# Kernel tuning notes

Measured on AMD Instinct MI355X. Metric: run time of the kernel, lower is better.

## Reference

```python
import jax, jax.numpy as jnp
import numpy as np

B, H, SQ, SKV, D = 2, 16, 2048, 2048, 64
SCALE = 8  # sqrt(head_dim)


def setup_inputs() -> dict:
    key = jax.random.key(0)
    kq, kk, kv, km = jax.random.split(key, 4)
    q = jax.random.normal(kq, (B, H, SQ, D), dtype=jnp.float32)
    k = jax.random.normal(kk, (B, H, SKV, D), dtype=jnp.float32)
    v = jax.random.normal(kv, (B, H, SKV, D), dtype=jnp.float32)
    mask = jax.random.normal(km, (1, 1, SQ, SKV), dtype=jnp.float32)
    return {"q": q, "k": k, "v": v, "mask": mask, "scale": SCALE}


def reference(q, k, v, mask, scale):
    # scores: [B, H, SQ, SKV]
    scores = jnp.einsum("bhqd,bhkd->bhqk", q, k) / scale
    scores = scores + mask  # broadcast additive mask
    probs = jax.nn.softmax(scores, axis=-1)
    # hidden: [B, H, SQ, D]
    return jnp.einsum("bhqk,bhkd->bhqd", probs, v)
```

## Files before the change

### kernel.cpp

```cpp
#include <hip/hip_runtime.h>
#include <hip/hip_bf16.h>

#define NB 2
#define NH 16
#define NSQ 2048
#define NSKV 2048
#define ND 64
#define NT (NSKV / 64)
#define LOG2E 1.4426950408889634f
#define BHSTRIDE (NSKV * ND)

typedef __attribute__((ext_vector_type(8))) short bf16x8;
typedef __attribute__((ext_vector_type(4))) float f32x4;
typedef __attribute__((address_space(1))) const unsigned gas_u32;
typedef __attribute__((address_space(3))) unsigned las_u32;

__device__ __forceinline__ short f2bf(float x) {
  union { float f; unsigned u; } c; c.f = x;
  unsigned r = c.u + 0x7fffu + ((c.u >> 16) & 1u);
  return (short)(r >> 16);
}
__device__ __forceinline__ unsigned pack_bf2(float lo, float hi) {
  union { __hip_bfloat162 h; unsigned u; } c;
  c.h = __float22bfloat162_rn(float2{lo, hi});
  return c.u;
}
__device__ __forceinline__ float u2f(unsigned u) {
  union { unsigned u; float f; } c; c.u = u; return c.f;
}
__device__ __forceinline__ float exp2_fast(float x) {
#if __has_builtin(__builtin_amdgcn_exp2f)
  return __builtin_amdgcn_exp2f(x);
#else
  return exp2f(x);
#endif
}

__device__ __forceinline__ int kvmap(int x) {
  return (x & 3) | (((x >> 4) & 1) << 2) | (((x >> 2) & 1) << 3)
       | (((x >> 3) & 1) << 4) | (x & 32);
}

__global__ void prep_k(const float* __restrict__ K, short* __restrict__ Kp) {
  const int bh = blockIdx.y, tile = blockIdx.x, tid = (int)threadIdx.x;
#pragma unroll
  for (int h = 0; h < 2; ++h) {
    const int u    = tid + h * 256;
    const int nt   = u >> 7, kc = (u >> 6) & 1, lane = u & 63;
    const int prow = nt * 16 + (lane & 15);
    const float* src = K + ((size_t)bh * NSKV + tile * 64 + kvmap(prow)) * ND
                         + kc * 32 + (lane >> 4) * 8;
    float4 a = *(const float4*)src, b = *(const float4*)(src + 4);
    bf16x8 w;
    w[0]=f2bf(a.x); w[1]=f2bf(a.y); w[2]=f2bf(a.z); w[3]=f2bf(a.w);
    w[4]=f2bf(b.x); w[5]=f2bf(b.y); w[6]=f2bf(b.z); w[7]=f2bf(b.w);
    *(bf16x8*)(Kp + (size_t)bh * BHSTRIDE + (size_t)tile * 4096 + u * 8) = w;
  }
}

__global__ void prep_vt(const float* __restrict__ V, short* __restrict__ Vp) {
  __shared__ float T[64][65];
  const int kv0 = blockIdx.x * 64;
  const int bh  = blockIdx.y;
  const int t   = (int)threadIdx.x;
  const float* src = V + ((size_t)bh * NSKV + kv0) * ND;
#pragma unroll
  for (int i = 0; i < 4; ++i) {
    float4 v = *(const float4*)(src + (size_t)((t >> 4) + 16 * i) * ND + (t & 15) * 4);
    T[(t >> 4) + 16 * i][(t & 15) * 4 + 0] = v.x;
    T[(t >> 4) + 16 * i][(t & 15) * 4 + 1] = v.y;
    T[(t >> 4) + 16 * i][(t & 15) * 4 + 2] = v.z;
    T[(t >> 4) + 16 * i][(t & 15) * 4 + 3] = v.w;
  }
  __syncthreads();
  const int d = t >> 2, c = t & 3;
  bf16x8 w0, w1;
#pragma unroll
  for (int j = 0; j < 8; ++j) w0[j] = f2bf(T[c * 16 + j][d]);
#pragma unroll
  for (int j = 0; j < 8; ++j) w1[j] = f2bf(T[c * 16 + 8 + j][d]);
  const int frag  = (d >> 4) * 2 + (c >> 1);
  const int lane0 = (((2 * c) & 3) << 4) | (d & 15);
  const int lane1 = (((2 * c + 1) & 3) << 4) | (d & 15);
  short* dstb = Vp + (size_t)bh * BHSTRIDE + (size_t)blockIdx.x * 4096 + frag * 512;
  *(bf16x8*)(dstb + lane0 * 8) = w0;
  *(bf16x8*)(dstb + lane1 * 8) = w1;
}

__global__ void prep_mt(const float* __restrict__ M, unsigned short* __restrict__ Mt) {
  const int qt = blockIdx.x, kt = blockIdx.y, t = (int)threadIdx.x;
  const int rl = t >> 4, c = t & 15;
  const int row = qt * 16 + rl;
  float4 v = *(const float4*)(M + (size_t)row * NSKV + kt * 64 + c * 4);
  const int nt   = 2 * (c >> 3) + (c & 1);
  const int lq   = (c >> 1) & 3;
  const int lane = lq * 16 + rl;
  ushort4 o;
  o.x = (unsigned short)f2bf(LOG2E * v.x);
  o.y = (unsigned short)f2bf(LOG2E * v.y);
  o.z = (unsigned short)f2bf(LOG2E * v.z);
  o.w = (unsigned short)f2bf(LOG2E * v.w);
  *(ushort4*)(Mt + (((size_t)qt * 32 + kt) * 64 + lane) * 16 + nt * 4) = o;
}

__global__ __launch_bounds__(512, 4)
void attn_fwd(const float* __restrict__ Q, const short* __restrict__ Kp,
              const short* __restrict__ Vp, const unsigned short* __restrict__ Mt,
              const void* __restrict__ scale_p, float* __restrict__ O)
{
  const int lin = (int)blockIdx.x;
  const int j   = lin & 7, m = lin >> 3;
  const int qb  = 2 * j + (m & 1);
  const int bh  = m >> 1;

  const int tid = (int)threadIdx.x;
  const int wv  = tid >> 6;
  const int ln  = tid & 63;
  const int l16 = ln & 15;
  const int lq  = ln >> 4;

  float scale_v;
  {
    union { int i; float f; } u;
    u.i = ((const int*)scale_p)[0];
    float af = fabsf(u.f);
    scale_v = (af >= 1e-6f && af <= 1e6f) ? u.f : (float)u.i;
  }
  const float qmul = LOG2E / scale_v;

  const int q0 = qb * 128;
  const short* Kb = Kp + (size_t)bh * BHSTRIDE;
  const short* Vb = Vp + (size_t)bh * BHSTRIDE;

  __shared__ short Kl[2][4096];
  __shared__ short Vl[2][4096];

  bf16x8 qf[2];
  {
    const float* qrow = Q + ((size_t)bh * NSQ + q0 + wv * 16 + l16) * ND;
#pragma unroll
    for (int kc = 0; kc < 2; ++kc) {
      const float4* p = (const float4*)(qrow + kc * 32 + lq * 8);
      float4 a = p[0], b = p[1];
      bf16x8 f;
      f[0]=f2bf(a.x*qmul); f[1]=f2bf(a.y*qmul); f[2]=f2bf(a.z*qmul); f[3]=f2bf(a.w*qmul);
      f[4]=f2bf(b.x*qmul); f[5]=f2bf(b.y*qmul); f[6]=f2bf(b.z*qmul); f[7]=f2bf(b.w*qmul);
      qf[kc] = f;
    }
  }

  f32x4 oa[4];
  f32x4 lacc;
#pragma unroll
  for (int dt = 0; dt < 4; ++dt) { f32x4 z = {0.f,0.f,0.f,0.f}; oa[dt] = z; }
  { f32x4 z = {0.f,0.f,0.f,0.f}; lacc = z; }

  bf16x8 ones;
#pragma unroll
  for (int j2 = 0; j2 < 8; ++j2) ones[j2] = (short)0x3F80;

  const unsigned short* M0 = Mt + (size_t)(qb * 8 + wv) * 32768 + (size_t)ln * 16;

  union MU { uint4 q[2]; unsigned u[8]; };

  auto mload = [&](int t, MU& mu) {
    const unsigned short* p0 = M0 + (size_t)t * 1024;
    mu.q[0] = *(const uint4*)p0;
    mu.q[1] = *(const uint4*)(p0 + 8);
  };

  auto stage = [&](int t, int buf) {
    const short* ks = Kb + (size_t)t * 4096;
    const short* vs = Vb + (size_t)t * 4096;
    __builtin_amdgcn_global_load_lds((gas_u32*)(ks + wv * 512 + ln * 8),
                                     (las_u32*)&Kl[buf][wv * 512], 16, 0, 0);
    __builtin_amdgcn_global_load_lds((gas_u32*)(vs + wv * 512 + ln * 8),
                                     (las_u32*)&Vl[buf][wv * 512], 16, 0, 0);
  };

  auto tile = [&](int t, int buf, MU& mc, MU& mn) {
    if (t + 1 < NT) {
      stage(t + 1, buf ^ 1);
      mload(t + 1, mn);
    }
    bf16x8 kf[4][2], vf[4][2];
#pragma unroll
    for (int nt = 0; nt < 4; ++nt)
#pragma unroll
      for (int kc = 0; kc < 2; ++kc) {
        kf[nt][kc] = *(const bf16x8*)&Kl[buf][(nt * 2 + kc) * 512 + ln * 8];
        vf[nt][kc] = *(const bf16x8*)&Vl[buf][(nt * 2 + kc) * 512 + ln * 8];
      }
    f32x4 s[4];
    __builtin_amdgcn_s_setprio(1);
#pragma unroll
    for (int nt = 0; nt < 4; ++nt) {
      const unsigned w0 = mc.u[nt * 2], w1 = mc.u[nt * 2 + 1];
      f32x4 a;
      a[0] = u2f(w0 << 16); a[1] = u2f(w0 & 0xffff0000u);
      a[2] = u2f(w1 << 16); a[3] = u2f(w1 & 0xffff0000u);
      a = __builtin_amdgcn_mfma_f32_16x16x32_bf16(kf[nt][0], qf[0], a, 0, 0, 0);
      a = __builtin_amdgcn_mfma_f32_16x16x32_bf16(kf[nt][1], qf[1], a, 0, 0, 0);
      s[nt] = a;
    }
    __builtin_amdgcn_s_setprio(0);
#pragma unroll
    for (int nt = 0; nt < 4; ++nt) {
      s[nt][0] = exp2_fast(s[nt][0]);
      s[nt][1] = exp2_fast(s[nt][1]);
      s[nt][2] = exp2_fast(s[nt][2]);
      s[nt][3] = exp2_fast(s[nt][3]);
    }
    bf16x8 pa[2];
#pragma unroll
    for (int kc = 0; kc < 2; ++kc) {
      union { unsigned u[4]; bf16x8 v; } w;
      w.u[0] = pack_bf2(s[2*kc][0],   s[2*kc][1]);
      w.u[1] = pack_bf2(s[2*kc][2],   s[2*kc][3]);
      w.u[2] = pack_bf2(s[2*kc+1][0], s[2*kc+1][1]);
      w.u[3] = pack_bf2(s[2*kc+1][2], s[2*kc+1][3]);
      pa[kc] = w.v;
    }
    __builtin_amdgcn_s_setprio(1);
#pragma unroll
    for (int kc = 0; kc < 2; ++kc) {
#pragma unroll
      for (int dt = 0; dt < 4; ++dt)
        oa[dt] = __builtin_amdgcn_mfma_f32_16x16x32_bf16(pa[kc], vf[dt][kc], oa[dt], 0, 0, 0);
      lacc = __builtin_amdgcn_mfma_f32_16x16x32_bf16(pa[kc], ones, lacc, 0, 0, 0);
    }
    __builtin_amdgcn_s_setprio(0);
    __syncthreads();
  };

  MU mA, mB;
  stage(0, 0);
  mload(0, mA);
  __syncthreads();

  for (int t = 0; t < NT; t += 2) {
    tile(t,     0, mA, mB);
    tile(t + 1, 1, mB, mA);
  }

#pragma unroll
  for (int r = 0; r < 4; ++r) {
    const float inv = 1.0f / lacc[r];
    float* orow = O + ((size_t)bh * NSQ + q0 + wv * 16 + lq * 4 + r) * ND;
#pragma unroll
    for (int dt = 0; dt < 4; ++dt)
      orow[dt * 16 + l16] = oa[dt][r] * inv;
  }
}

extern "C" void kernel_launch(void* const* d_in, const int* in_sizes, int n_in,
                              void* d_out, int out_size, void* d_ws, size_t ws_size,
                              hipStream_t stream) {
  const float* q     = (const float*)d_in[0];
  const float* k     = (const float*)d_in[1];
  const float* v     = (const float*)d_in[2];
  const float* mask  = (const float*)d_in[3];
  const void*  scale = (const void*)d_in[4];
  float* out = (float*)d_out;

  const size_t NELEM = (size_t)NB * NH * NSKV * ND;
  short* Kpk = (short*)d_ws;
  short* Vpk = Kpk + NELEM;
  unsigned short* Mtl = (unsigned short*)(Vpk + NELEM);

  prep_k<<<dim3(NSKV / 64, NB * NH), 256, 0, stream>>>(k, Kpk);
  prep_vt<<<dim3(NSKV / 64, NB * NH), 256, 0, stream>>>(v, Vpk);
  prep_mt<<<dim3(NSQ / 16, NSKV / 64), 256, 0, stream>>>(mask, Mtl);

  attn_fwd<<<dim3(512), 512, 0, stream>>>(q, Kpk, Vpk, Mtl, scale, out);
}
```

Before: 77.87 us.

## Process two KV tiles per barrier and swizzle block-to-head mapping

```diff
diff --git a/kernel.cpp b/kernel.cpp
--- a/kernel.cpp
+++ b/kernel.cpp
@@ -109,9 +109,9 @@
               const void* __restrict__ scale_p, float* __restrict__ O)
 {
   const int lin = (int)blockIdx.x;
-  const int j   = lin & 7, m = lin >> 3;
-  const int qb  = 2 * j + (m & 1);
-  const int bh  = m >> 1;
+  const int swz = ((lin & 7) << 6) | (lin >> 3);
+  const int qb  = swz & 15;
+  const int bh  = swz >> 4;
 
   const int tid = (int)threadIdx.x;
   const int wv  = tid >> 6;
@@ -132,8 +132,8 @@
   const short* Kb = Kp + (size_t)bh * BHSTRIDE;
   const short* Vb = Vp + (size_t)bh * BHSTRIDE;
 
-  __shared__ short Kl[2][4096];
-  __shared__ short Vl[2][4096];
+  __shared__ short Kl[2][2][4096];
+  __shared__ short Vl[2][2][4096];
 
   bf16x8 qf[2];
   {
@@ -169,27 +169,25 @@
     mu.q[1] = *(const uint4*)(p0 + 8);
   };
 
-  auto stage = [&](int t, int buf) {
-    const short* ks = Kb + (size_t)t * 4096;
-    const short* vs = Vb + (size_t)t * 4096;
-    __builtin_amdgcn_global_load_lds((gas_u32*)(ks + wv * 512 + ln * 8),
-                                     (las_u32*)&Kl[buf][wv * 512], 16, 0, 0);
-    __builtin_amdgcn_global_load_lds((gas_u32*)(vs + wv * 512 + ln * 8),
-                                     (las_u32*)&Vl[buf][wv * 512], 16, 0, 0);
-  };
-
-  auto tile = [&](int t, int buf, MU& mc, MU& mn) {
-    if (t + 1 < NT) {
-      stage(t + 1, buf ^ 1);
-      mload(t + 1, mn);
-    }
+  auto stage = [&](int t2, int pair) {
+#pragma unroll
+    for (int tt = 0; tt < 2; ++tt) {
+      const int t = 2 * t2 + tt;
+      __builtin_amdgcn_global_load_lds((gas_u32*)(Kb + (size_t)t * 4096 + wv * 512 + ln * 8),
+                                       (las_u32*)&Kl[pair][tt][wv * 512], 16, 0, 0);
+      __builtin_amdgcn_global_load_lds((gas_u32*)(Vb + (size_t)t * 4096 + wv * 512 + ln * 8),
+                                       (las_u32*)&Vl[pair][tt][wv * 512], 16, 0, 0);
+    }
+  };
+
+  auto subtile = [&](int pair, int tt, MU& mc) {
     bf16x8 kf[4][2], vf[4][2];
 #pragma unroll
     for (int nt = 0; nt < 4; ++nt)
 #pragma unroll
       for (int kc = 0; kc < 2; ++kc) {
-        kf[nt][kc] = *(const bf16x8*)&Kl[buf][(nt * 2 + kc) * 512 + ln * 8];
-        vf[nt][kc] = *(const bf16x8*)&Vl[buf][(nt * 2 + kc) * 512 + ln * 8];
+        kf[nt][kc] = *(const bf16x8*)&Kl[pair][tt][(nt * 2 + kc) * 512 + ln * 8];
+        vf[nt][kc] = *(const bf16x8*)&Vl[pair][tt][(nt * 2 + kc) * 512 + ln * 8];
       }
     f32x4 s[4];
     __builtin_amdgcn_s_setprio(1);
@@ -230,17 +228,28 @@
       lacc = __builtin_amdgcn_mfma_f32_16x16x32_bf16(pa[kc], ones, lacc, 0, 0, 0);
     }
     __builtin_amdgcn_s_setprio(0);
+  };
+
+  auto iter = [&](int t2, int pair, MU (&mc)[2], MU (&mn)[2]) {
+    if (t2 + 1 < NT / 2) {
+      stage(t2 + 1, pair ^ 1);
+      mload(2 * t2 + 2, mn[0]);
+      mload(2 * t2 + 3, mn[1]);
+    }
+    subtile(pair, 0, mc[0]);
+    subtile(pair, 1, mc[1]);
     __syncthreads();
   };
 
-  MU mA, mB;
+  MU mA[2], mB[2];
   stage(0, 0);
-  mload(0, mA);
+  mload(0, mA[0]);
+  mload(1, mA[1]);
   __syncthreads();
 
-  for (int t = 0; t < NT; t += 2) {
-    tile(t,     0, mA, mB);
-    tile(t + 1, 1, mB, mA);
+  for (int t2 = 0; t2 < NT / 2; t2 += 2) {
+    iter(t2,     0, mA, mB);
+    iter(t2 + 1, 1, mB, mA);
   }
 
 #pragma unroll
```

After: 92.35 us. +18.6%, slower.
